# Optimization experiments

Hardware: AMD Instinct MI355X
Metric: run time of the kernel (lower is better)

## Reference

```python
import jax, jax.numpy as jnp
import numpy as np

B, S, HID, H = 2, 2048, 1024, 16
D_HEAD = HID // H  # 64
EPS = 1e-5


def _gammas():
    lo, hi = np.log(1.0 / 512.0), np.log(1.0 / 32.0)
    return (1.0 - np.exp(np.linspace(lo, hi, H))).astype(np.float32)


def _decay_mask():
    # D[h, n, m] = gamma_h^(n-m) for n >= m else 0  (causal exponential decay)
    gam = jnp.asarray(_gammas())                      # [H]
    pos = jnp.arange(S, dtype=jnp.float32)
    diff = pos[:, None] - pos[None, :]                # [S, S]
    keep = diff >= 0
    logg = jnp.log(gam)[:, None, None]                # [H,1,1]
    safe = jnp.where(keep, diff, 0.0)[None]           # avoid inf for masked entries
    return jnp.where(keep[None], jnp.exp(safe * logg), 0.0)  # [H, S, S]


def setup_inputs() -> dict:
    key = jax.random.key(0)
    ks = jax.random.split(key, 10)
    rn = lambda k, shape, s=1.0: jax.random.normal(k, shape, dtype=jnp.float32) * s
    return {
        "x": rn(ks[0], (B, S, HID)),
        "wq": rn(ks[1], (H, D_HEAD, D_HEAD), 1.0 / np.sqrt(D_HEAD)),
        "bq": rn(ks[2], (H, D_HEAD), 0.02),
        "wk": rn(ks[3], (H, D_HEAD, D_HEAD), 1.0 / np.sqrt(D_HEAD)),
        "bk": rn(ks[4], (H, D_HEAD), 0.02),
        "wv": rn(ks[5], (H, D_HEAD, D_HEAD), 1.0 / np.sqrt(D_HEAD)),
        "theta": rn(ks[6], (H, D_HEAD), 1.0 / D_HEAD),
        "gn_weight": jnp.ones((HID,), jnp.float32),
        "gn_bias": jnp.zeros((HID,), jnp.float32),
        "weight1": rn(ks[7], (HID, HID), 1.0 / HID),
        "weight2": rn(ks[8], (HID, HID), 1.0 / HID),
    }


def reference(x, wq, bq, wk, bk, wv, theta, gn_weight, gn_bias, weight1, weight2):
    # Per-head retention (all heads vectorized; torch loops over heads).
    xh = x.reshape(B, S, H, D_HEAD)
    q = jnp.einsum('bshd,hde->bshe', xh, wq) + bq
    k = jnp.einsum('bshd,hde->bshe', xh, wk) + bk
    v = jnp.einsum('bshd,hde->bshe', xh, wv)
    # Complex rotary factors exp(i*n*theta) on q, conj on k -> real part of q k^H:
    ang = jnp.arange(S, dtype=jnp.float32)[:, None, None] * theta[None]  # [S,H,d]
    cs, sn = jnp.cos(ang), jnp.sin(ang)
    scores = (jnp.einsum('bshd,bthd->bhst', q * cs, k * cs)
              + jnp.einsum('bshd,bthd->bhst', q * sn, k * sn))  # Re(QK^H) [B,H,S,S]
    scores = scores * _decay_mask()[None]                        # decay mask
    ret = jnp.einsum('bhst,bthd->bshd', scores, v)               # [B,S,H,d]
    # GroupNorm with groups = n_heads over channels (per-head normalization).
    mean = jnp.mean(ret, axis=-1, keepdims=True)
    var = jnp.var(ret, axis=-1, keepdims=True)
    retn = (ret - mean) * jax.lax.rsqrt(var + EPS)
    retn = retn.reshape(B, S, HID) * gn_weight + gn_bias
    # Swish gate on x @ W1, residual add, project with W2.
    gate = x @ weight1
    out = gate * jax.nn.sigmoid(gate) + retn
    return out @ weight2
```

## Files before the change

### kernel.cpp

```cpp
#include <hip/hip_runtime.h>
#include <cstdint>
#include <cstddef>

#define B_ 2
#define S_ 2048
#define HID_ 1024
#define H_ 16
#define DH_ 64

typedef __attribute__((ext_vector_type(8))) short short8;
typedef __attribute__((ext_vector_type(8))) unsigned short ushort8;
typedef __attribute__((ext_vector_type(4))) unsigned short ushort4v;
typedef __attribute__((ext_vector_type(4))) float floatx4;
typedef __attribute__((ext_vector_type(4))) float float4v;

static __device__ __forceinline__ unsigned short f2bf(float f) {
  unsigned int u = __float_as_uint(f);
  u += 0x7fffu + ((u >> 16) & 1u);
  return (unsigned short)(u >> 16);
}
static __device__ __forceinline__ float bf2f(unsigned short h) {
  return __uint_as_float(((unsigned int)h) << 16);
}

__global__ __launch_bounds__(256) void convert_kernel(
    const float* __restrict__ x, const float* __restrict__ w1,
    const float* __restrict__ w2, unsigned short* __restrict__ x_bf,
    unsigned short* __restrict__ w1t, unsigned short* __restrict__ w2t_hi,
    unsigned short* __restrict__ w2t_lo) {
  const int NX = B_ * S_ * HID_;
  const int NW = HID_ * HID_;
  int idx = blockIdx.x * 256 + threadIdx.x;
  if (idx < NX) {
    x_bf[idx] = f2bf(x[idx]);
  } else if (idx < NX + NW) {
    int i = idx - NX;
    int n = i >> 10, k = i & 1023;
    w1t[i] = f2bf(w1[k * HID_ + n]);
  } else if (idx < NX + 2 * NW) {
    int i = idx - NX - NW;
    int n = i >> 10, k = i & 1023;
    float v = w2[k * HID_ + n];
    unsigned short h = f2bf(v);
    w2t_hi[i] = h;
    w2t_lo[i] = f2bf(v - bf2f(h));
  }
}

__global__ __launch_bounds__(256) void qkv_kernel(
    const float* __restrict__ x, const float* __restrict__ wq,
    const float* __restrict__ bq, const float* __restrict__ wk,
    const float* __restrict__ bk, const float* __restrict__ wv,
    const float* __restrict__ theta,
    unsigned short* __restrict__ q_h, unsigned short* __restrict__ q_l,
    unsigned short* __restrict__ k_h, unsigned short* __restrict__ k_l,
    unsigned short* __restrict__ v_th, unsigned short* __restrict__ v_tl,
    int b) {
  __shared__ __align__(16) float xs[64 * 68];
  __shared__ __align__(16) float wqs[64 * 68];
  __shared__ __align__(16) float wks[64 * 68];
  __shared__ __align__(16) float wvs[64 * 68];

  int tid = threadIdx.x;
  int st = blockIdx.x, h = blockIdx.y;
  int s0 = st * 64;

#pragma unroll
  for (int i = 0; i < 4; ++i) {
    int cid = tid + i * 256;
    int r = cid >> 4, c4 = (cid & 15) * 4;
    *reinterpret_cast<float4v*>(&xs[r * 68 + c4]) =
        *reinterpret_cast<const float4v*>(x + ((size_t)(b * S_ + s0 + r)) * HID_ + h * DH_ + c4);
  }
#pragma unroll
  for (int i = 0; i < 4; ++i) {
    int cid = tid + i * 256;
    int d = cid >> 4, c4 = (cid & 15) * 4;
    *reinterpret_cast<float4v*>(&wqs[d * 68 + c4]) =
        *reinterpret_cast<const float4v*>(wq + (size_t)(h * DH_ + d) * DH_ + c4);
    *reinterpret_cast<float4v*>(&wks[d * 68 + c4]) =
        *reinterpret_cast<const float4v*>(wk + (size_t)(h * DH_ + d) * DH_ + c4);
    *reinterpret_cast<float4v*>(&wvs[d * 68 + c4]) =
        *reinterpret_cast<const float4v*>(wv + (size_t)(h * DH_ + d) * DH_ + c4);
  }
  __syncthreads();

  int rg = tid >> 3;
  int cg = tid & 7;
  int r0 = rg * 2, c0 = cg * 8;

  float aq[2][8], ak[2][8], av[2][8];
#pragma unroll
  for (int i = 0; i < 2; ++i)
#pragma unroll
    for (int j = 0; j < 8; ++j) { aq[i][j] = 0.f; ak[i][j] = 0.f; av[i][j] = 0.f; }

  for (int d = 0; d < 64; ++d) {
    float x0 = xs[(r0 + 0) * 68 + d];
    float x1 = xs[(r0 + 1) * 68 + d];
#pragma unroll
    for (int j = 0; j < 8; ++j) {
      float wqv = wqs[d * 68 + c0 + j];
      float wkv = wks[d * 68 + c0 + j];
      float wvv = wvs[d * 68 + c0 + j];
      aq[0][j] += x0 * wqv; aq[1][j] += x1 * wqv;
      ak[0][j] += x0 * wkv; ak[1][j] += x1 * wkv;
      av[0][j] += x0 * wvv; av[1][j] += x1 * wvv;
    }
  }

  float thv[8], bqv[8], bkv[8];
#pragma unroll
  for (int j = 0; j < 8; ++j) {
    thv[j] = theta[h * DH_ + c0 + j];
    bqv[j] = bq[h * DH_ + c0 + j];
    bkv[j] = bk[h * DH_ + c0 + j];
  }

  __syncthreads();
  unsigned short* VtH = reinterpret_cast<unsigned short*>(xs);
  unsigned short* VtL = reinterpret_cast<unsigned short*>(wqs);

#pragma unroll
  for (int i = 0; i < 2; ++i) {
    int s = s0 + r0 + i;
    size_t qb = ((size_t)h * S_ + s) * 128;
    ushort8 qch, qcl, qsh, qsl, kch, kcl, ksh, ksl;
#pragma unroll
    for (int j = 0; j < 8; ++j) {
      float q = aq[i][j] + bqv[j];
      float k = ak[i][j] + bkv[j];
      float ang = (float)s * thv[j];
      float cs = cosf(ang), sn = sinf(ang);
      float qc = q * cs, qs = q * sn;
      unsigned short hq1 = f2bf(qc);
      qch[j] = hq1;
      qcl[j] = f2bf(qc - bf2f(hq1));
      unsigned short hq2 = f2bf(qs);
      qsh[j] = hq2;
      qsl[j] = f2bf(qs - bf2f(hq2));
      float kc = k * cs, ksn = k * sn;
      unsigned short h1 = f2bf(kc);
      kch[j] = h1;
      kcl[j] = f2bf(kc - bf2f(h1));
      unsigned short h2 = f2bf(ksn);
      ksh[j] = h2;
      ksl[j] = f2bf(ksn - bf2f(h2));
      float vv = av[i][j];
      unsigned short vh1 = f2bf(vv);
      VtH[(c0 + j) * 72 + (r0 + i)] = vh1;
      VtL[(c0 + j) * 72 + (r0 + i)] = f2bf(vv - bf2f(vh1));
    }
    *reinterpret_cast<ushort8*>(q_h + qb + c0) = qch;
    *reinterpret_cast<ushort8*>(q_h + qb + 64 + c0) = qsh;
    *reinterpret_cast<ushort8*>(q_l + qb + c0) = qcl;
    *reinterpret_cast<ushort8*>(q_l + qb + 64 + c0) = qsl;
    *reinterpret_cast<ushort8*>(k_h + qb + c0) = kch;
    *reinterpret_cast<ushort8*>(k_h + qb + 64 + c0) = ksh;
    *reinterpret_cast<ushort8*>(k_l + qb + c0) = kcl;
    *reinterpret_cast<ushort8*>(k_l + qb + 64 + c0) = ksl;
  }
  __syncthreads();
#pragma unroll
  for (int i = 0; i < 2; ++i) {
    int cid = tid + i * 256;
    int d = cid >> 3, t8 = (cid & 7) * 8;
    size_t gb = ((size_t)(h * 64 + d)) * S_ + s0 + t8;
    *reinterpret_cast<ushort8*>(v_th + gb) = *reinterpret_cast<const ushort8*>(&VtH[d * 72 + t8]);
    *reinterpret_cast<ushort8*>(v_tl + gb) = *reinterpret_cast<const ushort8*>(&VtL[d * 72 + t8]);
  }
}

#define SCOFF(row, colb)   ((row) * 256 + ((colb) ^ (((row) & 7) << 4)))

__global__ __launch_bounds__(256) void retention_split_kernel(
    const unsigned short* __restrict__ q_h, const unsigned short* __restrict__ q_l,
    const unsigned short* __restrict__ k_h, const unsigned short* __restrict__ k_l,
    const unsigned short* __restrict__ v_th, const unsigned short* __restrict__ v_tl,
    float* __restrict__ partial) {
  __shared__ __align__(16) unsigned short Kh[64 * 128];
  __shared__ __align__(16) unsigned short Kl[64 * 128];
  __shared__ __align__(16) unsigned short Vh[64 * 64];
  __shared__ __align__(16) unsigned short Vl[64 * 64];
  __shared__ __align__(16) float Sc[64 * 64];

  char* KhB = (char*)Kh;
  char* KlB = (char*)Kl;
  char* VhB = (char*)Vh;
  char* VlB = (char*)Vl;
  char* ScB = (char*)Sc;

  int tid = threadIdx.x;
  int w = tid >> 6;
  int lane = tid & 63, ln = lane & 15, quad = lane >> 4;
  int wr = w >> 1, wc = w & 1;
  int f = blockIdx.x;
  int h = ((f & 7) << 1) | ((f >> 3) & 1);
  int half = (f >> 4) & 1;
  int qt = 31 - (f >> 5);
  int s0 = qt * 64;

  int m = (qt + 2) >> 1;
  int kt0 = half ? m : 0;
  int kt1 = half ? (qt + 1) : m;

  const float lo_c = -6.2383246250395075f, hi_c = -3.4657359027997265f;
  float gam = 1.f - __expf(lo_c + (hi_c - lo_c) * ((float)h * (1.f / 15.f)));
  float logg = __logf(gam);

  float rowf[2][4], colf[2];
#pragma unroll
  for (int rt = 0; rt < 2; ++rt)
#pragma unroll
    for (int rr = 0; rr < 4; ++rr)
      rowf[rt][rr] = __expf((float)(wr * 32 + rt * 16 + quad * 4 + rr) * logg);
#pragma unroll
  for (int ns = 0; ns < 2; ++ns)
    colf[ns] = __expf(-(float)(wc * 32 + ns * 16 + ln) * logg);

  const unsigned short* khb = k_h + (size_t)h * S_ * 128;
  const unsigned short* klb = k_l + (size_t)h * S_ * 128;
  const unsigned short* vhb = v_th + (size_t)h * 64 * S_;
  const unsigned short* vlb = v_tl + (size_t)h * 64 * S_;

  short8 qfh[2][4], qfl[2][4];
#pragma unroll
  for (int rt = 0; rt < 2; ++rt) {
    int sQ = s0 + wr * 32 + rt * 16 + ln;
    const unsigned short* qhp = q_h + ((size_t)h * S_ + sQ) * 128 + quad * 8;
    const unsigned short* qlp = q_l + ((size_t)h * S_ + sQ) * 128 + quad * 8;
#pragma unroll
    for (int c = 0; c < 4; ++c) {
      qfh[rt][c] = *reinterpret_cast<const short8*>(qhp + c * 32);
      qfl[rt][c] = *reinterpret_cast<const short8*>(qlp + c * 32);
    }
  }

  floatx4 accO[4];
#pragma unroll
  for (int i = 0; i < 4; ++i) accO[i] = (floatx4){0.f, 0.f, 0.f, 0.f};

  ushort8 skh[4], skl[4], svh[2], svl[2];
  {
    int t00 = kt0 * 64;
#pragma unroll
    for (int i = 0; i < 4; ++i) {
      int cid = tid + i * 256;
      int r = cid >> 4, c8 = (cid & 15) * 8;
      skh[i] = *reinterpret_cast<const ushort8*>(khb + ((size_t)(t00 + r)) * 128 + c8);
      skl[i] = *reinterpret_cast<const ushort8*>(klb + ((size_t)(t00 + r)) * 128 + c8);
    }
#pragma unroll
    for (int i = 0; i < 2; ++i) {
      int cid = tid + i * 256;
      int d = cid >> 3, t8 = (cid & 7) * 8;
      svh[i] = *reinterpret_cast<const ushort8*>(vhb + (size_t)d * S_ + t00 + t8);
      svl[i] = *reinterpret_cast<const ushort8*>(vlb + (size_t)d * S_ + t00 + t8);
    }
#pragma unroll
    for (int i = 0; i < 4; ++i) {
      int cid = tid + i * 256;
      int r = cid >> 4;
      int ko = r * 256 + (((cid & 15) * 16) ^ ((r & 7) << 4));
      *reinterpret_cast<ushort8*>(KhB + ko) = skh[i];
      *reinterpret_cast<ushort8*>(KlB + ko) = skl[i];
    }
#pragma unroll
    for (int i = 0; i < 2; ++i) {
      int cid = tid + i * 256;
      int d = cid >> 3;
      int vo = d * 128 + (((cid & 7) * 16) ^ ((d & 7) << 4));
      *reinterpret_cast<ushort8*>(VhB + vo) = svh[i];
      *reinterpret_cast<ushort8*>(VlB + vo) = svl[i];
    }
    if (kt0 + 1 < kt1) {
      int t01 = (kt0 + 1) * 64;
#pragma unroll
      for (int i = 0; i < 4; ++i) {
        int cid = tid + i * 256;
        int r = cid >> 4, c8 = (cid & 15) * 8;
        skh[i] = *reinterpret_cast<const ushort8*>(khb + ((size_t)(t01 + r)) * 128 + c8);
        skl[i] = *reinterpret_cast<const ushort8*>(klb + ((size_t)(t01 + r)) * 128 + c8);
      }
#pragma unroll
      for (int i = 0; i < 2; ++i) {
        int cid = tid + i * 256;
        int d = cid >> 3, t8 = (cid & 7) * 8;
        svh[i] = *reinterpret_cast<const ushort8*>(vhb + (size_t)d * S_ + t01 + t8);
        svl[i] = *reinterpret_cast<const ushort8*>(vlb + (size_t)d * S_ + t01 + t8);
      }
    }
  }
  __syncthreads();

  for (int kt = kt0; kt < kt1; ++kt) {
    floatx4 accS[2][2];
#pragma unroll
    for (int rt = 0; rt < 2; ++rt)
#pragma unroll
      for (int ns = 0; ns < 2; ++ns) accS[rt][ns] = (floatx4){0.f, 0.f, 0.f, 0.f};
#pragma unroll
    for (int ns = 0; ns < 2; ++ns) {
      int krow = wc * 32 + ns * 16 + ln;
#pragma unroll
      for (int ks = 0; ks < 4; ++ks) {
        int off = krow * 256 + ((ks * 64 + quad * 16) ^ ((ln & 7) << 4));
        short8 kh = *reinterpret_cast<const short8*>(KhB + off);
        short8 kl = *reinterpret_cast<const short8*>(KlB + off);
#pragma unroll
        for (int rt = 0; rt < 2; ++rt) {
          accS[rt][ns] = __builtin_amdgcn_mfma_f32_16x16x32_bf16(qfh[rt][ks], kh, accS[rt][ns], 0, 0, 0);
          accS[rt][ns] = __builtin_amdgcn_mfma_f32_16x16x32_bf16(qfl[rt][ks], kh, accS[rt][ns], 0, 0, 0);
          accS[rt][ns] = __builtin_amdgcn_mfma_f32_16x16x32_bf16(qfh[rt][ks], kl, accS[rt][ns], 0, 0, 0);
        }
      }
    }

    float tf = __expf((float)(64 * (qt - kt)) * logg);
    float trf[2][4];
#pragma unroll
    for (int rt = 0; rt < 2; ++rt)
#pragma unroll
      for (int rr = 0; rr < 4; ++rr) trf[rt][rr] = tf * rowf[rt][rr];
    if (kt < qt) {
#pragma unroll
      for (int rt = 0; rt < 2; ++rt)
#pragma unroll
        for (int ns = 0; ns < 2; ++ns) {
          int col = wc * 32 + ns * 16 + ln;
#pragma unroll
          for (int rr = 0; rr < 4; ++rr) {
            int row = wr * 32 + rt * 16 + quad * 4 + rr;
            *reinterpret_cast<float*>(ScB + SCOFF(row, col * 4)) =
                accS[rt][ns][rr] * trf[rt][rr] * colf[ns];
          }
        }
    } else {
#pragma unroll
      for (int rt = 0; rt < 2; ++rt)
#pragma unroll
        for (int ns = 0; ns < 2; ++ns) {
          int col = wc * 32 + ns * 16 + ln;
#pragma unroll
          for (int rr = 0; rr < 4; ++rr) {
            int row = wr * 32 + rt * 16 + quad * 4 + rr;
            float v = accS[rt][ns][rr] * trf[rt][rr] * colf[ns];
            *reinterpret_cast<float*>(ScB + SCOFF(row, col * 4)) =
                (row >= col) ? v : 0.f;
          }
        }
    }
    __syncthreads();

#pragma unroll
    for (int ks = 0; ks < 2; ++ks) {
      int prw = w * 16 + ln;
      int cb = ks * 128 + quad * 32;
      float4v p0 = *reinterpret_cast<const float4v*>(ScB + SCOFF(prw, cb));
      float4v p1 = *reinterpret_cast<const float4v*>(ScB + SCOFF(prw, cb + 16));
      short8 ph, pl;
#pragma unroll
      for (int j = 0; j < 4; ++j) {
        unsigned short hh = f2bf(p0[j]);
        ph[j] = (short)hh;
        pl[j] = (short)f2bf(p0[j] - bf2f(hh));
        unsigned short hh2 = f2bf(p1[j]);
        ph[4 + j] = (short)hh2;
        pl[4 + j] = (short)f2bf(p1[j] - bf2f(hh2));
      }
#pragma unroll
      for (int ds = 0; ds < 4; ++ds) {
        int d = ds * 16 + ln;
        int voff = d * 128 + ((ks * 64 + quad * 16) ^ ((ln & 7) << 4));
        short8 vh = *reinterpret_cast<const short8*>(VhB + voff);
        short8 vl = *reinterpret_cast<const short8*>(VlB + voff);
        accO[ds] = __builtin_amdgcn_mfma_f32_16x16x32_bf16(ph, vh, accO[ds], 0, 0, 0);
        accO[ds] = __builtin_amdgcn_mfma_f32_16x16x32_bf16(pl, vh, accO[ds], 0, 0, 0);
        accO[ds] = __builtin_amdgcn_mfma_f32_16x16x32_bf16(ph, vl, accO[ds], 0, 0, 0);
      }
    }

    __syncthreads();
    if (kt + 1 < kt1) {
#pragma unroll
      for (int i = 0; i < 4; ++i) {
        int cid = tid + i * 256;
        int r = cid >> 4;
        int ko = r * 256 + (((cid & 15) * 16) ^ ((r & 7) << 4));
        *reinterpret_cast<ushort8*>(KhB + ko) = skh[i];
        *reinterpret_cast<ushort8*>(KlB + ko) = skl[i];
      }
#pragma unroll
      for (int i = 0; i < 2; ++i) {
        int cid = tid + i * 256;
        int d = cid >> 3;
        int vo = d * 128 + (((cid & 7) * 16) ^ ((d & 7) << 4));
        *reinterpret_cast<ushort8*>(VhB + vo) = svh[i];
        *reinterpret_cast<ushort8*>(VlB + vo) = svl[i];
      }
      if (kt + 2 < kt1) {
        int t0n = (kt + 2) * 64;
#pragma unroll
        for (int i = 0; i < 4; ++i) {
          int cid = tid + i * 256;
          int r = cid >> 4, c8 = (cid & 15) * 8;
          skh[i] = *reinterpret_cast<const ushort8*>(khb + ((size_t)(t0n + r)) * 128 + c8);
          skl[i] = *reinterpret_cast<const ushort8*>(klb + ((size_t)(t0n + r)) * 128 + c8);
        }
#pragma unroll
        for (int i = 0; i < 2; ++i) {
          int cid = tid + i * 256;
          int d = cid >> 3, t8 = (cid & 7) * 8;
          svh[i] = *reinterpret_cast<const ushort8*>(vhb + (size_t)d * S_ + t0n + t8);
          svl[i] = *reinterpret_cast<const ushort8*>(vlb + (size_t)d * S_ + t0n + t8);
        }
      }
      __syncthreads();
    }
  }

  float* pout = partial + ((size_t)(((h * 32 + qt) << 1) + half)) * 4096;
#pragma unroll
  for (int ds = 0; ds < 4; ++ds) {
#pragma unroll
    for (int rr = 0; rr < 4; ++rr) {
      pout[(w * 16 + quad * 4 + rr) * 64 + ds * 16 + ln] = accO[ds][rr];
    }
  }
}

__global__ __launch_bounds__(256) void combine_gn_kernel(
    const float* __restrict__ partial, const float* __restrict__ gn_w,
    const float* __restrict__ gn_b, float* __restrict__ retn, int b) {
  __shared__ float gnred[64][8];
  int tid = threadIdx.x;
  int qi = blockIdx.x;
  int h = qi >> 5, qt = qi & 31;
  const float* p0 = partial + (size_t)qi * 8192;
  const float* p1 = p0 + 4096;

  int r2 = tid >> 2;
  int sub = tid & 3;
  float a16[16];
#pragma unroll
  for (int c = 0; c < 4; ++c) {
    int o = r2 * 64 + sub * 16 + c * 4;
    float4v va = *reinterpret_cast<const float4v*>(p0 + o);
    float4v vb = *reinterpret_cast<const float4v*>(p1 + o);
#pragma unroll
    for (int j = 0; j < 4; ++j) a16[c * 4 + j] = va[j] + vb[j];
  }

  float psum = 0.f, psq = 0.f;
#pragma unroll
  for (int i = 0; i < 16; ++i) { psum += a16[i]; psq += a16[i] * a16[i]; }
  gnred[r2][sub] = psum;
  gnred[r2][4 + sub] = psq;
  float sum = gnred[r2][0] + gnred[r2][1] + gnred[r2][2] + gnred[r2][3];
  float sq = gnred[r2][4] + gnred[r2][5] + gnred[r2][6] + gnred[r2][7];
  float mean = sum * (1.f / 64.f);
  float var = sq * (1.f / 64.f) - mean * mean;
  float rstd = rsqrtf(var + 1e-5f);

  size_t obase = ((size_t)(b * S_ + qt * 64 + r2)) * HID_ + h * DH_ + sub * 16;
#pragma unroll
  for (int i = 0; i < 16; ++i) {
    float gw = gn_w[h * DH_ + sub * 16 + i];
    float gb = gn_b[h * DH_ + sub * 16 + i];
    retn[obase + i] = (a16[i] - mean) * rstd * gw + gb;
  }
}

__global__ __launch_bounds__(256) void gemm_gate_kernel(
    const unsigned short* __restrict__ A, const unsigned short* __restrict__ Bt,
    const float* __restrict__ retn, unsigned short* __restrict__ pre_hi,
    unsigned short* __restrict__ pre_lo) {
  const int K = HID_;
  __shared__ __align__(16) unsigned short Al[128 * 56];
  __shared__ __align__(16) unsigned short Bl[64 * 56];

  int tid = threadIdx.x;
  int lane = tid & 63, ln = lane & 15, quad = lane >> 4;
  int w = tid >> 6, wm = w >> 1, wn = w & 1;
  int m0 = blockIdx.y * 128, n0 = blockIdx.x * 64;

  floatx4 acc[4][2];
#pragma unroll
  for (int i = 0; i < 4; ++i)
#pragma unroll
    for (int j = 0; j < 2; ++j) acc[i][j] = (floatx4){0.f, 0.f, 0.f, 0.f};

  for (int k0 = 0; k0 < K; k0 += 32) {
    __syncthreads();
#pragma unroll
    for (int i = 0; i < 2; ++i) {
      int cid = tid + i * 256;
      int r = cid >> 2, c8 = (cid & 3) * 8;
      *reinterpret_cast<ushort8*>(&Al[r * 56 + c8]) =
          *reinterpret_cast<const ushort8*>(A + (size_t)(m0 + r) * K + k0 + c8);
    }
    {
      int r = tid >> 2, c8 = (tid & 3) * 8;
      *reinterpret_cast<ushort8*>(&Bl[r * 56 + c8]) =
          *reinterpret_cast<const ushort8*>(Bt + (size_t)(n0 + r) * K + k0 + c8);
    }
    __syncthreads();

    short8 af[4], bfr[2];
#pragma unroll
    for (int i = 0; i < 4; ++i)
      af[i] = *reinterpret_cast<const short8*>(&Al[(wm * 64 + i * 16 + ln) * 56 + quad * 8]);
#pragma unroll
    for (int i = 0; i < 2; ++i)
      bfr[i] = *reinterpret_cast<const short8*>(&Bl[(wn * 32 + i * 16 + ln) * 56 + quad * 8]);
#pragma unroll
    for (int mi = 0; mi < 4; ++mi)
#pragma unroll
      for (int ni = 0; ni < 2; ++ni)
        acc[mi][ni] = __builtin_amdgcn_mfma_f32_16x16x32_bf16(af[mi], bfr[ni], acc[mi][ni], 0, 0, 0);
  }

#pragma unroll
  for (int mi = 0; mi < 4; ++mi) {
#pragma unroll
    for (int r = 0; r < 4; ++r) {
      int row = m0 + wm * 64 + mi * 16 + quad * 4 + r;
#pragma unroll
      for (int ni = 0; ni < 2; ++ni) {
        int col = n0 + wn * 32 + ni * 16 + ln;
        float g = acc[mi][ni][r];
        float val = g * (1.f / (1.f + __expf(-g))) + retn[(size_t)row * HID_ + col];
        unsigned short hh = f2bf(val);
        size_t oidx = (size_t)row * HID_ + col;
        pre_hi[oidx] = hh;
        pre_lo[oidx] = f2bf(val - bf2f(hh));
      }
    }
  }
}

__global__ __launch_bounds__(256) void gemm_out_kernel(
    const unsigned short* __restrict__ Ah, const unsigned short* __restrict__ Alo,
    const unsigned short* __restrict__ Bth, const unsigned short* __restrict__ Btlo,
    float* __restrict__ out_f) {
  const int K = HID_;
  __shared__ __align__(16) unsigned short AhS[128 * 56];
  __shared__ __align__(16) unsigned short AlS[128 * 56];
  __shared__ __align__(16) unsigned short BhS[64 * 56];
  __shared__ __align__(16) unsigned short BlS[64 * 56];

  int tid = threadIdx.x;
  int lane = tid & 63, ln = lane & 15, quad = lane >> 4;
  int w = tid >> 6, wm = w >> 1, wn = w & 1;
  int m0 = blockIdx.y * 128, n0 = blockIdx.x * 64;

  floatx4 acc[4][2];
#pragma unroll
  for (int i = 0; i < 4; ++i)
#pragma unroll
    for (int j = 0; j < 2; ++j) acc[i][j] = (floatx4){0.f, 0.f, 0.f, 0.f};

  for (int k0 = 0; k0 < K; k0 += 32) {
    __syncthreads();
#pragma unroll
    for (int i = 0; i < 2; ++i) {
      int cid = tid + i * 256;
      int r = cid >> 2, c8 = (cid & 3) * 8;
      size_t ga = (size_t)(m0 + r) * K + k0 + c8;
      *reinterpret_cast<ushort8*>(&AhS[r * 56 + c8]) = *reinterpret_cast<const ushort8*>(Ah + ga);
      *reinterpret_cast<ushort8*>(&AlS[r * 56 + c8]) = *reinterpret_cast<const ushort8*>(Alo + ga);
    }
    {
      int r = tid >> 2, c8 = (tid & 3) * 8;
      size_t gb = (size_t)(n0 + r) * K + k0 + c8;
      *reinterpret_cast<ushort8*>(&BhS[r * 56 + c8]) = *reinterpret_cast<const ushort8*>(Bth + gb);
      *reinterpret_cast<ushort8*>(&BlS[r * 56 + c8]) = *reinterpret_cast<const ushort8*>(Btlo + gb);
    }
    __syncthreads();

    short8 afh[4], afl[4], bfh[2], bfl[2];
#pragma unroll
    for (int i = 0; i < 4; ++i) {
      int ao = (wm * 64 + i * 16 + ln) * 56 + quad * 8;
      afh[i] = *reinterpret_cast<const short8*>(&AhS[ao]);
      afl[i] = *reinterpret_cast<const short8*>(&AlS[ao]);
    }
#pragma unroll
    for (int i = 0; i < 2; ++i) {
      int bo = (wn * 32 + i * 16 + ln) * 56 + quad * 8;
      bfh[i] = *reinterpret_cast<const short8*>(&BhS[bo]);
      bfl[i] = *reinterpret_cast<const short8*>(&BlS[bo]);
    }
#pragma unroll
    for (int mi = 0; mi < 4; ++mi)
#pragma unroll
      for (int ni = 0; ni < 2; ++ni) {
        floatx4 a = acc[mi][ni];
        a = __builtin_amdgcn_mfma_f32_16x16x32_bf16(afh[mi], bfh[ni], a, 0, 0, 0);
        a = __builtin_amdgcn_mfma_f32_16x16x32_bf16(afl[mi], bfh[ni], a, 0, 0, 0);
        a = __builtin_amdgcn_mfma_f32_16x16x32_bf16(afh[mi], bfl[ni], a, 0, 0, 0);
        acc[mi][ni] = a;
      }
  }

#pragma unroll
  for (int mi = 0; mi < 4; ++mi) {
#pragma unroll
    for (int r = 0; r < 4; ++r) {
      int row = m0 + wm * 64 + mi * 16 + quad * 4 + r;
#pragma unroll
      for (int ni = 0; ni < 2; ++ni) {
        int col = n0 + wn * 32 + ni * 16 + ln;
        out_f[(size_t)row * HID_ + col] = acc[mi][ni][r];
      }
    }
  }
}

extern "C" void kernel_launch(void* const* d_in, const int* in_sizes, int n_in,
                              void* d_out, int out_size, void* d_ws,
                              size_t ws_size, hipStream_t stream) {
  (void)in_sizes; (void)n_in; (void)out_size; (void)ws_size;
  const float* x = (const float*)d_in[0];
  const float* wq = (const float*)d_in[1];
  const float* bq = (const float*)d_in[2];
  const float* wk = (const float*)d_in[3];
  const float* bk = (const float*)d_in[4];
  const float* wv = (const float*)d_in[5];
  const float* theta = (const float*)d_in[6];
  const float* gn_w = (const float*)d_in[7];
  const float* gn_b = (const float*)d_in[8];
  const float* w1 = (const float*)d_in[9];
  const float* w2 = (const float*)d_in[10];

  const size_t MB = 1024 * 1024;
  char* ws = (char*)d_ws;
  unsigned short* x_bf   = (unsigned short*)(ws + 0 * MB);
  unsigned short* w1t    = (unsigned short*)(ws + 8 * MB);
  unsigned short* w2t_hi = (unsigned short*)(ws + 10 * MB);
  unsigned short* w2t_lo = (unsigned short*)(ws + 12 * MB);
  unsigned short* q_h    = (unsigned short*)(ws + 14 * MB);
  unsigned short* q_l    = (unsigned short*)(ws + 22 * MB);
  unsigned short* k_h    = (unsigned short*)(ws + 30 * MB);
  unsigned short* k_l    = (unsigned short*)(ws + 38 * MB);
  unsigned short* v_th   = (unsigned short*)(ws + 46 * MB);
  unsigned short* v_tl   = (unsigned short*)(ws + 50 * MB);
  float*          retn   = (float*)(ws + 54 * MB);
  float*          partial= (float*)(ws + 70 * MB);
  unsigned short* pre_hi = (unsigned short*)(ws + 14 * MB);
  unsigned short* pre_lo = (unsigned short*)(ws + 22 * MB);
  float* out = (float*)d_out;

  convert_kernel<<<dim3(24576), 256, 0, stream>>>(x, w1, w2, x_bf, w1t, w2t_hi, w2t_lo);
  for (int b = 0; b < B_; ++b) {
    qkv_kernel<<<dim3(S_ / 64, H_), 256, 0, stream>>>(
        x, wq, bq, wk, bk, wv, theta, q_h, q_l, k_h, k_l, v_th, v_tl, b);
    retention_split_kernel<<<dim3(1024), 256, 0, stream>>>(
        q_h, q_l, k_h, k_l, v_th, v_tl, partial);
    combine_gn_kernel<<<dim3(512), 256, 0, stream>>>(
        partial, gn_w, gn_b, retn, b);
  }
  gemm_gate_kernel<<<dim3(HID_ / 64, (B_ * S_) / 128), 256, 0, stream>>>(
      x_bf, w1t, retn, pre_hi, pre_lo);
  gemm_out_kernel<<<dim3(HID_ / 64, (B_ * S_) / 128), 256, 0, stream>>>(
      pre_hi, pre_lo, w2t_hi, w2t_lo, out);
}
```

Before: 338.0 us.

## Double-buffer V tile in retention and register-prefetch GEMM operand loads

In the retention kernel, V gets two shared-memory buffers. The next K and V tiles are written to shared memory, and the following tile is prefetched from global, right after the score barrier. This overlaps that work with the P·V MFMA phase and removes one barrier per iteration. Both GEMM kernels now prefetch the next k-slice of A and B into registers before the MFMA loop, so global load latency is hidden behind compute. The cost is more shared memory and register pressure, which may reduce occupancy.

```diff
diff --git a/kernel.cpp b/kernel.cpp
--- a/kernel.cpp
+++ b/kernel.cpp
@@ -180,8 +180,8 @@
     float* __restrict__ partial) {
   __shared__ __align__(16) unsigned short Kh[64 * 128];
   __shared__ __align__(16) unsigned short Kl[64 * 128];
-  __shared__ __align__(16) unsigned short Vh[64 * 64];
-  __shared__ __align__(16) unsigned short Vl[64 * 64];
+  __shared__ __align__(16) unsigned short Vh[2][64 * 64];
+  __shared__ __align__(16) unsigned short Vl[2][64 * 64];
   __shared__ __align__(16) float Sc[64 * 64];
 
   char* KhB = (char*)Kh;
@@ -294,6 +294,7 @@
   __syncthreads();
 
   for (int kt = kt0; kt < kt1; ++kt) {
+    int vb = (kt - kt0) & 1;
     floatx4 accS[2][2];
 #pragma unroll
     for (int rt = 0; rt < 2; ++rt)
@@ -352,6 +353,42 @@
     }
     __syncthreads();
 
+    if (kt + 1 < kt1) {
+#pragma unroll
+      for (int i = 0; i < 4; ++i) {
+        int cid = tid + i * 256;
+        int r = cid >> 4;
+        int ko = r * 256 + (((cid & 15) * 16) ^ ((r & 7) << 4));
+        *reinterpret_cast<ushort8*>(KhB + ko) = skh[i];
+        *reinterpret_cast<ushort8*>(KlB + ko) = skl[i];
+      }
+#pragma unroll
+      for (int i = 0; i < 2; ++i) {
+        int cid = tid + i * 256;
+        int d = cid >> 3;
+        int vo = (vb ^ 1) * 8192 + d * 128 + (((cid & 7) * 16) ^ ((d & 7) << 4));
+        *reinterpret_cast<ushort8*>(VhB + vo) = svh[i];
+        *reinterpret_cast<ushort8*>(VlB + vo) = svl[i];
+      }
+      if (kt + 2 < kt1) {
+        int t0n = (kt + 2) * 64;
+#pragma unroll
+        for (int i = 0; i < 4; ++i) {
+          int cid = tid + i * 256;
+          int r = cid >> 4, c8 = (cid & 15) * 8;
+          skh[i] = *reinterpret_cast<const ushort8*>(khb + ((size_t)(t0n + r)) * 128 + c8);
+          skl[i] = *reinterpret_cast<const ushort8*>(klb + ((size_t)(t0n + r)) * 128 + c8);
+        }
+#pragma unroll
+        for (int i = 0; i < 2; ++i) {
+          int cid = tid + i * 256;
+          int d = cid >> 3, t8 = (cid & 7) * 8;
+          svh[i] = *reinterpret_cast<const ushort8*>(vhb + (size_t)d * S_ + t0n + t8);
+          svl[i] = *reinterpret_cast<const ushort8*>(vlb + (size_t)d * S_ + t0n + t8);
+        }
+      }
+    }
+
 #pragma unroll
     for (int ks = 0; ks < 2; ++ks) {
       int prw = w * 16 + ln;
@@ -371,7 +408,7 @@
 #pragma unroll
       for (int ds = 0; ds < 4; ++ds) {
         int d = ds * 16 + ln;
-        int voff = d * 128 + ((ks * 64 + quad * 16) ^ ((ln & 7) << 4));
+        int voff = vb * 8192 + d * 128 + ((ks * 64 + quad * 16) ^ ((ln & 7) << 4));
         short8 vh = *reinterpret_cast<const short8*>(VhB + voff);
         short8 vl = *reinterpret_cast<const short8*>(VlB + voff);
         accO[ds] = __builtin_amdgcn_mfma_f32_16x16x32_bf16(ph, vh, accO[ds], 0, 0, 0);
@@ -381,42 +418,6 @@
     }
 
     __syncthreads();
-    if (kt + 1 < kt1) {
-#pragma unroll
-      for (int i = 0; i < 4; ++i) {
-        int cid = tid + i * 256;
-        int r = cid >> 4;
-        int ko = r * 256 + (((cid & 15) * 16) ^ ((r & 7) << 4));
-        *reinterpret_cast<ushort8*>(KhB + ko) = skh[i];
-        *reinterpret_cast<ushort8*>(KlB + ko) = skl[i];
-      }
-#pragma unroll
-      for (int i = 0; i < 2; ++i) {
-        int cid = tid + i * 256;
-        int d = cid >> 3;
-        int vo = d * 128 + (((cid & 7) * 16) ^ ((d & 7) << 4));
-        *reinterpret_cast<ushort8*>(VhB + vo) = svh[i];
-        *reinterpret_cast<ushort8*>(VlB + vo) = svl[i];
-      }
-      if (kt + 2 < kt1) {
-        int t0n = (kt + 2) * 64;
-#pragma unroll
-        for (int i = 0; i < 4; ++i) {
-          int cid = tid + i * 256;
-          int r = cid >> 4, c8 = (cid & 15) * 8;
-          skh[i] = *reinterpret_cast<const ushort8*>(khb + ((size_t)(t0n + r)) * 128 + c8);
-          skl[i] = *reinterpret_cast<const ushort8*>(klb + ((size_t)(t0n + r)) * 128 + c8);
-        }
-#pragma unroll
-        for (int i = 0; i < 2; ++i) {
-          int cid = tid + i * 256;
-          int d = cid >> 3, t8 = (cid & 7) * 8;
-          svh[i] = *reinterpret_cast<const ushort8*>(vhb + (size_t)d * S_ + t0n + t8);
-          svl[i] = *reinterpret_cast<const ushort8*>(vlb + (size_t)d * S_ + t0n + t8);
-        }
-      }
-      __syncthreads();
-    }
   }
 
   float* pout = partial + ((size_t)(((h * 32 + qt) << 1) + half)) * 4096;
@@ -490,19 +491,30 @@
 #pragma unroll
     for (int j = 0; j < 2; ++j) acc[i][j] = (floatx4){0.f, 0.f, 0.f, 0.f};
 
+  int ra_r[2], ra_c[2], rb_r, rb_c;
+#pragma unroll
+  for (int i = 0; i < 2; ++i) {
+    int cid = tid + i * 256;
+    ra_r[i] = cid >> 2; ra_c[i] = (cid & 3) * 8;
+  }
+  rb_r = tid >> 2; rb_c = (tid & 3) * 8;
+
+  ushort8 ra[2], rb;
+#pragma unroll
+  for (int i = 0; i < 2; ++i)
+    ra[i] = *reinterpret_cast<const ushort8*>(A + (size_t)(m0 + ra_r[i]) * K + ra_c[i]);
+  rb = *reinterpret_cast<const ushort8*>(Bt + (size_t)(n0 + rb_r) * K + rb_c);
+
   for (int k0 = 0; k0 < K; k0 += 32) {
-    __syncthreads();
-#pragma unroll
-    for (int i = 0; i < 2; ++i) {
-      int cid = tid + i * 256;
-      int r = cid >> 2, c8 = (cid & 3) * 8;
-      *reinterpret_cast<ushort8*>(&Al[r * 56 + c8]) =
-          *reinterpret_cast<const ushort8*>(A + (size_t)(m0 + r) * K + k0 + c8);
-    }
-    {
-      int r = tid >> 2, c8 = (tid & 3) * 8;
-      *reinterpret_cast<ushort8*>(&Bl[r * 56 + c8]) =
-          *reinterpret_cast<const ushort8*>(Bt + (size_t)(n0 + r) * K + k0 + c8);
+#pragma unroll
+    for (int i = 0; i < 2; ++i)
+      *reinterpret_cast<ushort8*>(&Al[ra_r[i] * 56 + ra_c[i]]) = ra[i];
+    *reinterpret_cast<ushort8*>(&Bl[rb_r * 56 + rb_c]) = rb;
+    if (k0 + 32 < K) {
+#pragma unroll
+      for (int i = 0; i < 2; ++i)
+        ra[i] = *reinterpret_cast<const ushort8*>(A + (size_t)(m0 + ra_r[i]) * K + k0 + 32 + ra_c[i]);
+      rb = *reinterpret_cast<const ushort8*>(Bt + (size_t)(n0 + rb_r) * K + k0 + 32 + rb_c);
     }
     __syncthreads();
 
@@ -518,6 +530,7 @@
 #pragma unroll
       for (int ni = 0; ni < 2; ++ni)
         acc[mi][ni] = __builtin_amdgcn_mfma_f32_16x16x32_bf16(af[mi], bfr[ni], acc[mi][ni], 0, 0, 0);
+    __syncthreads();
   }
 
 #pragma unroll
@@ -560,21 +573,45 @@
 #pragma unroll
     for (int j = 0; j < 2; ++j) acc[i][j] = (floatx4){0.f, 0.f, 0.f, 0.f};
 
+  int ra_r[2], ra_c[2], rb_r, rb_c;
+#pragma unroll
+  for (int i = 0; i < 2; ++i) {
+    int cid = tid + i * 256;
+    ra_r[i] = cid >> 2; ra_c[i] = (cid & 3) * 8;
+  }
+  rb_r = tid >> 2; rb_c = (tid & 3) * 8;
+
+  ushort8 rah[2], ral[2], rbh, rbl;
+#pragma unroll
+  for (int i = 0; i < 2; ++i) {
+    size_t ga = (size_t)(m0 + ra_r[i]) * K + ra_c[i];
+    rah[i] = *reinterpret_cast<const ushort8*>(Ah + ga);
+    ral[i] = *reinterpret_cast<const ushort8*>(Alo + ga);
+  }
+  {
+    size_t gb = (size_t)(n0 + rb_r) * K + rb_c;
+    rbh = *reinterpret_cast<const ushort8*>(Bth + gb);
+    rbl = *reinterpret_cast<const ushort8*>(Btlo + gb);
+  }
+
   for (int k0 = 0; k0 < K; k0 += 32) {
-    __syncthreads();
 #pragma unroll
     for (int i = 0; i < 2; ++i) {
-      int cid = tid + i * 256;
-      int r = cid >> 2, c8 = (cid & 3) * 8;
-      size_t ga = (size_t)(m0 + r) * K + k0 + c8;
-      *reinterpret_cast<ushort8*>(&AhS[r * 56 + c8]) = *reinterpret_cast<const ushort8*>(Ah + ga);
-      *reinterpret_cast<ushort8*>(&AlS[r * 56 + c8]) = *reinterpret_cast<const ushort8*>(Alo + ga);
-    }
-    {
-      int r = tid >> 2, c8 = (tid & 3) * 8;
-      size_t gb = (size_t)(n0 + r) * K + k0 + c8;
-      *reinterpret_cast<ushort8*>(&BhS[r * 56 + c8]) = *reinterpret_cast<const ushort8*>(Bth + gb);
-      *reinterpret_cast<ushort8*>(&BlS[r * 56 + c8]) = *reinterpret_cast<const ushort8*>(Btlo + gb);
+      *reinterpret_cast<ushort8*>(&AhS[ra_r[i] * 56 + ra_c[i]]) = rah[i];
+      *reinterpret_cast<ushort8*>(&AlS[ra_r[i] * 56 + ra_c[i]]) = ral[i];
+    }
+    *reinterpret_cast<ushort8*>(&BhS[rb_r * 56 + rb_c]) = rbh;
+    *reinterpret_cast<ushort8*>(&BlS[rb_r * 56 + rb_c]) = rbl;
+    if (k0 + 32 < K) {
+#pragma unroll
+      for (int i = 0; i < 2; ++i) {
+        size_t ga = (size_t)(m0 + ra_r[i]) * K + k0 + 32 + ra_c[i];
+        rah[i] = *reinterpret_cast<const ushort8*>(Ah + ga);
+        ral[i] = *reinterpret_cast<const ushort8*>(Alo + ga);
+      }
+      size_t gb = (size_t)(n0 + rb_r) * K + k0 + 32 + rb_c;
+      rbh = *reinterpret_cast<const ushort8*>(Bth + gb);
+      rbl = *reinterpret_cast<const ushort8*>(Btlo + gb);
     }
     __syncthreads();
 
@@ -601,6 +638,7 @@
         a = __builtin_amdgcn_mfma_f32_16x16x32_bf16(afh[mi], bfl[ni], a, 0, 0, 0);
         acc[mi][ni] = a;
       }
+    __syncthreads();
   }
 
 #pragma unroll
```

After: 330.7 us. 1.02x faster.
